# Optimization experiments

Hardware: AMD Instinct MI355X
Metric: run time of the kernel (lower is better)

## Reference

```python
import jax, jax.numpy as jnp
import numpy as np

B, S, H = 2, 2048, 2048
N_HEADS, N_KV, HEAD_DIM = 16, 8, 128
EPS = 1e-6
ROPE_THETA = 1e6


def _rms_norm(x, w, eps=EPS):
    # per-head RMSNorm over last dim (head_dim), computed in fp32
    xf = x.astype(jnp.float32)
    var = jnp.mean(xf * xf, axis=-1, keepdims=True)
    return (w * (xf * jax.lax.rsqrt(var + eps))).astype(x.dtype)


def _rotate_half(x):
    x1, x2 = jnp.split(x, 2, axis=-1)
    return jnp.concatenate((-x2, x1), axis=-1)


def setup_inputs() -> dict:
    key = jax.random.key(0)
    ks = jax.random.split(key, 6)
    hidden_states = jax.random.normal(ks[0], (B, S, H), dtype=jnp.float32)
    # RoPE tables: [B, S, head_dim]
    inv_freq = 1.0 / (ROPE_THETA ** (np.arange(0, HEAD_DIM, 2, dtype=np.float32) / HEAD_DIM))
    pos = np.arange(S, dtype=np.float32)
    freqs = np.outer(pos, inv_freq)                      # [S, head_dim/2]
    emb = np.concatenate([freqs, freqs], axis=-1)        # [S, head_dim]
    cos = jnp.broadcast_to(jnp.asarray(np.cos(emb)), (B, S, HEAD_DIM))
    sin = jnp.broadcast_to(jnp.asarray(np.sin(emb)), (B, S, HEAD_DIM))
    # additive causal mask [B, 1, S, S]
    causal = jnp.triu(jnp.full((S, S), -1e9, dtype=jnp.float32), k=1)
    attention_mask = jnp.broadcast_to(causal[None, None], (B, 1, S, S))
    scale = 0.02
    Wq = jax.random.normal(ks[1], (N_HEADS * HEAD_DIM, H), dtype=jnp.float32) * scale
    Wk = jax.random.normal(ks[2], (N_KV * HEAD_DIM, H), dtype=jnp.float32) * scale
    Wv = jax.random.normal(ks[3], (N_KV * HEAD_DIM, H), dtype=jnp.float32) * scale
    Wo = jax.random.normal(ks[4], (H, N_HEADS * HEAD_DIM), dtype=jnp.float32) * scale
    q_norm_w = jnp.ones((HEAD_DIM,), dtype=jnp.float32)
    k_norm_w = jnp.ones((HEAD_DIM,), dtype=jnp.float32)
    return dict(hidden_states=hidden_states, cos=cos, sin=sin,
                attention_mask=attention_mask, Wq=Wq, Wk=Wk, Wv=Wv, Wo=Wo,
                q_norm_w=q_norm_w, k_norm_w=k_norm_w)


def reference(hidden_states, cos, sin, attention_mask, Wq, Wk, Wv, Wo, q_norm_w, k_norm_w):
    b, s, _ = hidden_states.shape
    scaling = HEAD_DIM ** -0.5
    n_rep = N_HEADS // N_KV
    # QKV projections (torch Linear: x @ W.T), split into heads
    q = jnp.einsum('bsh,dh->bsd', hidden_states, Wq).reshape(b, s, N_HEADS, HEAD_DIM)
    k = jnp.einsum('bsh,dh->bsd', hidden_states, Wk).reshape(b, s, N_KV, HEAD_DIM)
    v = jnp.einsum('bsh,dh->bsd', hidden_states, Wv).reshape(b, s, N_KV, HEAD_DIM)
    # per-head QK RMSNorm, then [B, H, S, D]
    q = _rms_norm(q, q_norm_w).transpose(0, 2, 1, 3)
    k = _rms_norm(k, k_norm_w).transpose(0, 2, 1, 3)
    v = v.transpose(0, 2, 1, 3)
    # RoPE (cos/sin unsqueezed over head dim)
    c = cos[:, None, :, :]
    sn = sin[:, None, :, :]
    q = q * c + _rotate_half(q) * sn
    k = k * c + _rotate_half(k) * sn
    # GQA: repeat kv heads
    k = jnp.repeat(k, n_rep, axis=1)
    v = jnp.repeat(v, n_rep, axis=1)
    # eager attention: materialize full [B, H, S, S] scores
    attn_weights = jnp.einsum('bhqd,bhkd->bhqk', q, k) * scaling + attention_mask
    attn_weights = jax.nn.softmax(attn_weights.astype(jnp.float32), axis=-1).astype(q.dtype)
    attn_output = jnp.einsum('bhqk,bhkd->bhqd', attn_weights, v)
    attn_output = attn_output.transpose(0, 2, 1, 3).reshape(b, s, N_HEADS * HEAD_DIM)
    attn_output = jnp.einsum('bsd,hd->bsh', attn_output, Wo)
    return attn_output, attn_weights
```

## Files before the change

kernel.cpp:

```cpp
#include <hip/hip_runtime.h>
#include <stdint.h>

typedef unsigned short u16;
typedef __attribute__((ext_vector_type(8))) short bf16x8;
typedef __attribute__((ext_vector_type(4))) float f32x4;
typedef __attribute__((ext_vector_type(4))) unsigned short u16x4;
typedef __attribute__((ext_vector_type(8))) unsigned short u16x8;

#define SCALE_LOG2E 0.12751743007633614f

__device__ __forceinline__ u16 f2bf(float x){
  uint32_t u = __float_as_uint(x);
  u += 0x7FFFu + ((u >> 16) & 1u);
  return (u16)(u >> 16);
}
__device__ __forceinline__ u16 f2bf_trunc(float x){
  return (u16)(__float_as_uint(x) >> 16);
}
__device__ __forceinline__ float bf2f(u16 h){
  return __uint_as_float(((uint32_t)h) << 16);
}
__device__ __forceinline__ void gload16(const void* g, void* l){
  __builtin_amdgcn_global_load_lds((const __attribute__((address_space(1))) void*)g,
                                   (__attribute__((address_space(3))) void*)l, 16, 0, 0);
}

__global__ __launch_bounds__(256) void k_cvt5(
    const float* __restrict__ s0, u16* __restrict__ d0,
    const float* __restrict__ s1, u16* __restrict__ d1,
    const float* __restrict__ s2, u16* __restrict__ d2,
    const float* __restrict__ s3, u16* __restrict__ d3,
    const float* __restrict__ s4, u16* __restrict__ d4)
{
  int b = blockIdx.x;
  const float* s; u16* d; int off;
  if      (b < 8192)  { s=s0; d=d0; off=b; }
  else if (b < 12288) { s=s1; d=d1; off=b-8192; }
  else if (b < 14336) { s=s2; d=d2; off=b-12288; }
  else if (b < 16384) { s=s3; d=d3; off=b-14336; }
  else                { s=s4; d=d4; off=b-16384; }
  size_t i = ((size_t)off * 256 + threadIdx.x) * 4;
  float4 v = *(const float4*)(s + i);
  ushort4 o;
  o.x = f2bf(v.x); o.y = f2bf(v.y); o.z = f2bf(v.z); o.w = f2bf(v.w);
  *(ushort4*)(d + i) = o;
}

#define STAGE_UNIT(PTR, ROWOFF, BUF, TENS, KS, T1) do{ \
  _Pragma("unroll") \
  for(int jj=0;jj<2;jj++){ \
    int rs_ = wid*32 + jj*16 + (lane>>2); \
    int kp_ = (lane&3) ^ ((rs_>>1)&3); \
    gload16((PTR) + (size_t)((ROWOFF)+rs_)*K + (size_t)(T1)*64 + (KS)*32 + kp_*8, \
            &lds[BUF][TENS][KS][(wid*2+jj)*512]); \
  }}while(0)

#define FRAG(BASE, ROW) (*(const bf16x8*)((BASE) + (ROW)*32 + ((c_ ^ (((ROW)>>1)&3))<<3)))

__global__ __launch_bounds__(512,2) void k_gemm256(
    const u16* __restrict__ A, const u16* __restrict__ Bw, void* __restrict__ Cout,
    int N, int K, int ldc, int out_f32)
{
  __shared__ u16 lds[2][2][2][256*32];
  const int tid = threadIdx.x, wid = tid>>6, lane = tid&63;
  const int nbn = N >> 8;
  const int cpx = gridDim.x >> 3;
  const int bid = (blockIdx.x & 7)*cpx + (blockIdx.x >> 3);
  const int bm = bid / nbn, bn = bid % nbn;
  const int m0 = bm<<8, n0 = bn<<8;
  const int wm = wid>>2, wn = wid&3;
  const int c_ = lane>>4, rl = lane&15;

  f32x4 acc[8][4];
  f32x4 zero4 = {0.f,0.f,0.f,0.f};
#pragma unroll
  for (int i=0;i<8;i++)
#pragma unroll
    for (int j=0;j<4;j++) acc[i][j] = zero4;

  STAGE_UNIT(A,  m0, 0, 0, 0, 0);
  STAGE_UNIT(Bw, n0, 0, 1, 0, 0);
  STAGE_UNIT(A,  m0, 0, 0, 1, 0);
  STAGE_UNIT(Bw, n0, 0, 1, 1, 0);

  const int nt = K >> 6;
#pragma unroll 2
  for (int t=0; t<nt; ++t) {
    const int cur = t&1, nxt = cur^1;
    const bool pf = (t+1 < nt);
    const u16* Ab0 = lds[cur][0][0];
    const u16* Bb0 = lds[cur][1][0];
    const u16* Ab1 = lds[cur][0][1];
    const u16* Bb1 = lds[cur][1][1];
    bf16x8 af[4], bf[4];

    asm volatile("s_waitcnt vmcnt(4)" ::: "memory");
    __builtin_amdgcn_s_barrier();
    asm volatile("" ::: "memory");
#pragma unroll
    for (int j=0;j<4;j++) bf[j] = FRAG(Bb0, wn*64 + j*16 + rl);
#pragma unroll
    for (int i=0;i<4;i++) af[i] = FRAG(Ab0, wm*128 + i*16 + rl);
    if (pf) STAGE_UNIT(A, m0, nxt, 0, 0, t+1);
    __builtin_amdgcn_s_setprio(1);
#pragma unroll
    for (int i=0;i<4;i++)
#pragma unroll
      for (int j=0;j<4;j++)
        acc[i][j] = __builtin_amdgcn_mfma_f32_16x16x32_bf16(af[i], bf[j], acc[i][j], 0,0,0);
    __builtin_amdgcn_s_setprio(0);
    __builtin_amdgcn_s_barrier();
    asm volatile("" ::: "memory");

#pragma unroll
    for (int i=0;i<4;i++) af[i] = FRAG(Ab0, wm*128 + (i+4)*16 + rl);
    if (pf) STAGE_UNIT(Bw, n0, nxt, 1, 0, t+1);
    __builtin_amdgcn_s_setprio(1);
#pragma unroll
    for (int i=0;i<4;i++)
#pragma unroll
      for (int j=0;j<4;j++)
        acc[i+4][j] = __builtin_amdgcn_mfma_f32_16x16x32_bf16(af[i], bf[j], acc[i+4][j], 0,0,0);
    __builtin_amdgcn_s_setprio(0);
    __builtin_amdgcn_s_barrier();
    asm volatile("" ::: "memory");

    if (pf) { asm volatile("s_waitcnt vmcnt(4)" ::: "memory"); }
    else    { asm volatile("s_waitcnt vmcnt(0)" ::: "memory"); }
    __builtin_amdgcn_s_barrier();
    asm volatile("" ::: "memory");
#pragma unroll
    for (int j=0;j<4;j++) bf[j] = FRAG(Bb1, wn*64 + j*16 + rl);
#pragma unroll
    for (int i=0;i<4;i++) af[i] = FRAG(Ab1, wm*128 + i*16 + rl);
    if (pf) STAGE_UNIT(A, m0, nxt, 0, 1, t+1);
    __builtin_amdgcn_s_setprio(1);
#pragma unroll
    for (int i=0;i<4;i++)
#pragma unroll
      for (int j=0;j<4;j++)
        acc[i][j] = __builtin_amdgcn_mfma_f32_16x16x32_bf16(af[i], bf[j], acc[i][j], 0,0,0);
    __builtin_amdgcn_s_setprio(0);
    __builtin_amdgcn_s_barrier();
    asm volatile("" ::: "memory");

#pragma unroll
    for (int i=0;i<4;i++) af[i] = FRAG(Ab1, wm*128 + (i+4)*16 + rl);
    if (pf) STAGE_UNIT(Bw, n0, nxt, 1, 1, t+1);
    __builtin_amdgcn_s_setprio(1);
#pragma unroll
    for (int i=0;i<4;i++)
#pragma unroll
      for (int j=0;j<4;j++)
        acc[i+4][j] = __builtin_amdgcn_mfma_f32_16x16x32_bf16(af[i], bf[j], acc[i+4][j], 0,0,0);
    __builtin_amdgcn_s_setprio(0);
    __builtin_amdgcn_s_barrier();
    asm volatile("" ::: "memory");
  }

  const int r0 = m0 + wm*128 + ((lane>>4)<<2);
  const int c0 = n0 + wn*64 + rl;
  if (out_f32) {
    float* C = (float*)Cout;
#pragma unroll
    for (int i=0;i<8;i++)
#pragma unroll
      for (int j=0;j<4;j++)
#pragma unroll
        for (int r=0;r<4;r++)
          C[(size_t)(r0 + i*16 + r)*ldc + (c0 + j*16)] = acc[i][j][r];
  } else {
    u16* C = (u16*)Cout;
#pragma unroll
    for (int i=0;i<8;i++)
#pragma unroll
      for (int j=0;j<4;j++)
#pragma unroll
        for (int r=0;r<4;r++)
          C[(size_t)(r0 + i*16 + r)*ldc + (c0 + j*16)] = f2bf(acc[i][j][r]);
  }
}

#define STAGE_A128(BUF, KS, T1) do{ \
  int rs_ = wid*16 + (lane>>2); \
  int kp_ = (lane&3) ^ ((rs_>>1)&3); \
  gload16(A + (size_t)(m0+rs_)*K + (size_t)(T1)*64 + (KS)*32 + kp_*8, \
          &ldsA[BUF][KS][wid*512]); \
  }while(0)

#define STAGE_B128(BUF, KS, T1) do{ \
  _Pragma("unroll") \
  for(int jj=0;jj<2;jj++){ \
    int rs_ = wid*32 + jj*16 + (lane>>2); \
    int kp_ = (lane&3) ^ ((rs_>>1)&3); \
    gload16(Bw + (size_t)(n0+rs_)*K + (size_t)(T1)*64 + (KS)*32 + kp_*8, \
            &ldsB[BUF][KS][(wid*2+jj)*512]); \
  }}while(0)

__global__ __launch_bounds__(512,2) void k_gemm_bm128(
    const u16* __restrict__ A, const u16* __restrict__ Bw, float* __restrict__ C,
    int N, int K, int ldc)
{
  __shared__ u16 ldsA[2][2][128*32];
  __shared__ u16 ldsB[2][2][256*32];
  const int tid = threadIdx.x, wid = tid>>6, lane = tid&63;
  const int nbn = N >> 8;
  const int cpx = gridDim.x >> 3;
  const int bid = (blockIdx.x & 7)*cpx + (blockIdx.x >> 3);
  const int bm = bid / nbn, bn = bid % nbn;
  const int m0 = bm<<7, n0 = bn<<8;
  const int wm = wid>>2, wn = wid&3;
  const int c_ = lane>>4, rl = lane&15;

  f32x4 acc[4][4];
  f32x4 zero4 = {0.f,0.f,0.f,0.f};
#pragma unroll
  for (int i=0;i<4;i++)
#pragma unroll
    for (int j=0;j<4;j++) acc[i][j] = zero4;

  STAGE_A128(0, 0, 0);
  STAGE_B128(0, 0, 0);
  STAGE_A128(0, 1, 0);
  STAGE_B128(0, 1, 0);

  const int nt = K >> 6;
#pragma unroll 2
  for (int t=0; t<nt; ++t) {
    const int cur = t&1, nxt = cur^1;
    const bool pf = (t+1 < nt);
    bf16x8 af[4], bf[4];

    asm volatile("s_waitcnt vmcnt(3)" ::: "memory");
    __builtin_amdgcn_s_barrier();
    asm volatile("" ::: "memory");
#pragma unroll
    for (int i=0;i<4;i++) af[i] = FRAG(ldsA[cur][0], wm*64 + i*16 + rl);
#pragma unroll
    for (int j=0;j<4;j++) bf[j] = FRAG(ldsB[cur][0], wn*64 + j*16 + rl);
    if (pf) { STAGE_A128(nxt, 0, t+1); STAGE_B128(nxt, 0, t+1); }
    __builtin_amdgcn_s_setprio(1);
#pragma unroll
    for (int i=0;i<4;i++)
#pragma unroll
      for (int j=0;j<4;j++)
        acc[i][j] = __builtin_amdgcn_mfma_f32_16x16x32_bf16(af[i], bf[j], acc[i][j], 0,0,0);
    __builtin_amdgcn_s_setprio(0);
    __builtin_amdgcn_s_barrier();
    asm volatile("" ::: "memory");

    if (pf) { asm volatile("s_waitcnt vmcnt(3)" ::: "memory"); }
    else    { asm volatile("s_waitcnt vmcnt(0)" ::: "memory"); }
    __builtin_amdgcn_s_barrier();
    asm volatile("" ::: "memory");
#pragma unroll
    for (int i=0;i<4;i++) af[i] = FRAG(ldsA[cur][1], wm*64 + i*16 + rl);
#pragma unroll
    for (int j=0;j<4;j++) bf[j] = FRAG(ldsB[cur][1], wn*64 + j*16 + rl);
    if (pf) { STAGE_A128(nxt, 1, t+1); STAGE_B128(nxt, 1, t+1); }
    __builtin_amdgcn_s_setprio(1);
#pragma unroll
    for (int i=0;i<4;i++)
#pragma unroll
      for (int j=0;j<4;j++)
        acc[i][j] = __builtin_amdgcn_mfma_f32_16x16x32_bf16(af[i], bf[j], acc[i][j], 0,0,0);
    __builtin_amdgcn_s_setprio(0);
    __builtin_amdgcn_s_barrier();
    asm volatile("" ::: "memory");
  }

  const int r0 = m0 + wm*64 + ((lane>>4)<<2);
  const int c0 = n0 + wn*64 + rl;
#pragma unroll
  for (int i=0;i<4;i++)
#pragma unroll
    for (int j=0;j<4;j++)
#pragma unroll
      for (int r=0;r<4;r++)
        C[(size_t)(r0 + i*16 + r)*ldc + (c0 + j*16)] = acc[i][j][r];
}

__global__ __launch_bounds__(256) void k_prep(
    u16* __restrict__ qkv, u16* __restrict__ vt,
    const float* __restrict__ cosb, const float* __restrict__ sinb,
    const float* __restrict__ kw)
{
  __shared__ u16 tile[64][72];
  const int tid = threadIdx.x;
  if (blockIdx.x < 8192) {
    const int lane = tid&63;
    const int task = blockIdx.x*4 + (tid>>6);
    const int bs = task >> 3, col = 2048 + (task & 7)*128;
    u16* row = qkv + (size_t)bs*4096 + col;
    float x0 = bf2f(row[lane]), x1 = bf2f(row[lane+64]);
    float ss = x0*x0 + x1*x1;
#pragma unroll
    for (int m=1; m<64; m<<=1) ss += __shfl_xor(ss, m, 64);
    float rn = rsqrtf(ss*(1.0f/128.0f) + 1e-6f);
    const float* cp = cosb + (size_t)bs*128;
    const float* sp = sinb + (size_t)bs*128;
    float q0 = x0*rn*kw[lane], q1 = x1*rn*kw[lane+64];
    float o0 = q0*cp[lane]    - q1*sp[lane];
    float o1 = q1*cp[lane+64] + q0*sp[lane+64];
    row[lane]    = f2bf(o0);
    row[lane+64] = f2bf(o1);
  } else {
    const int bid = blockIdx.x - 8192;
    const int dt = bid & 1, st = (bid>>1)&31, kvh = (bid>>6)&7, b = bid>>9;
    const int rr = tid >> 3, c = (tid & 7) * 8;
    const u16* src = qkv + ((size_t)(b*2048 + st*64))*4096 + 3072 + kvh*128 + dt*64;
#pragma unroll
    for (int p=0;p<2;p++){
      int sl = p*32 + rr;
      u16x8 v = *(const u16x8*)(src + (size_t)sl*4096 + c);
#pragma unroll
      for (int e=0;e<8;e++) tile[sl][c+e] = v[e];
    }
    __syncthreads();
    u16* dst = vt + ((size_t)((b*8+kvh)*128 + dt*64))*2048 + st*64;
#pragma unroll
    for (int p=0;p<2;p++){
      int dl = p*32 + rr;
      u16x8 o;
#pragma unroll
      for (int e=0;e<8;e++) o[e] = tile[c+e][dl];
      *(u16x8*)(dst + (size_t)dl*2048 + c) = o;
    }
  }
}

#define STAGE_K8(T, DSTBUF) do { \
  _Pragma("unroll") \
  for (int i_=0;i_<2;i_++){ \
    int r_ = wv*8 + i_*4 + (lane>>4); \
    int cs_ = (lane&15) ^ (r_&7); \
    gload16(Kb + (size_t)((T)*64 + r_)*4096 + cs_*8, (DSTBUF) + (wv*2+i_)*512); \
  } } while(0)

#define STAGE_V8(T, DSTBUF) do { \
  _Pragma("unroll") \
  for (int i_=0;i_<2;i_++){ \
    int d_ = wv*16 + i_*8 + (lane>>3); \
    int cs_ = (lane&7) ^ (d_&7); \
    gload16(Vb + (size_t)d_*2048 + (T)*64 + cs_*8, (DSTBUF) + (wv*2+i_)*512); \
  } } while(0)

#define COMPUTE_S16(SACC, KBUF) do { \
  _Pragma("unroll") \
  for (int ks_=0;ks_<4;ks_++){ \
    bf16x8 bfr_[4]; \
    _Pragma("unroll") \
    for (int ns_=0;ns_<4;ns_++){ \
      int n_ = ns_*16 + (lane&15); \
      int sl_ = (ks_*4 + (lane>>4)) ^ (n_&7); \
      bfr_[ns_] = *(const bf16x8*)((KBUF) + n_*128 + sl_*8); \
    } \
    _Pragma("unroll") \
    for (int ns_=0;ns_<4;ns_++) \
      SACC[ns_] = __builtin_amdgcn_mfma_f32_16x16x32_bf16(qf[ks_], bfr_[ns_], SACC[ns_], 0,0,0); \
  } } while(0)

__global__ __launch_bounds__(512,4) void k_attn(
    const u16* __restrict__ qkv, const u16* __restrict__ vt,
    const float* __restrict__ cosb, const float* __restrict__ sinb,
    const float* __restrict__ qw,
    float* __restrict__ probs, u16* __restrict__ attn_o)
{
  __shared__ u16 lKV[4][64*128];
  __shared__ u16 lP[8][16*64];
  const int tid = threadIdx.x, wv = tid>>6, lane = tid&63;
  const int rl = lane&15, hi = lane>>4;
  const int bid = blockIdx.x;
  const int r9 = bid >> 5;
  const int qt = (r9 < 8) ? (15 - r9) : (r9 - 8);
  const int bh = bid & 31;
  const int h = bh & 15, b = bh >> 4;
  const int kvh = h>>1;
  const int q0 = qt<<7;
  const u16* Qb = qkv + (size_t)b*2048*4096 + h*128;
  const u16* Kb = qkv + (size_t)b*2048*4096 + 2048 + kvh*128;
  const u16* Vb = vt + (size_t)(b*8+kvh)*128*2048;

  f32x4 zero4 = {0.f,0.f,0.f,0.f};

  const int nkt = 2*qt + 2;
  const int tdiag = 2*qt + (wv>>2);
  const int rb = q0 + wv*16 + hi*4;

  STAGE_K8(0, lKV[0]);
  STAGE_K8(1, lKV[1]);
  if (nkt > 2) STAGE_K8(2, lKV[2]);

  bf16x8 qf[4];
  {
    const int srow = q0 + wv*16 + rl;
    float xq[4][8];
    float ss = 0.f;
#pragma unroll
    for (int ks=0;ks<4;ks++){
      bf16x8 raw = *(const bf16x8*)(Qb + (size_t)srow*4096 + ks*32 + hi*8);
#pragma unroll
      for (int j=0;j<8;j++){
        float x = bf2f((u16)raw[j]);
        xq[ks][j] = x;
        ss += x*x;
      }
    }
    ss += __shfl_xor(ss, 16, 64);
    ss += __shfl_xor(ss, 32, 64);
    float rn = rsqrtf(ss*(1.0f/128.0f) + 1e-6f);
    const float* cp = cosb + (size_t)(b*2048 + srow)*128;
    const float* sp = sinb + (size_t)(b*2048 + srow)*128;
#pragma unroll
    for (int ks2=0;ks2<2;ks2++){
#pragma unroll
      for (int j=0;j<8;j++){
        int d0 = ks2*32 + hi*8 + j;
        int d1 = d0 + 64;
        float a  = xq[ks2][j]   * rn * qw[d0];
        float bb = xq[ks2+2][j] * rn * qw[d1];
        float o0 = a*cp[d0] - bb*sp[d0];
        float o1 = bb*cp[d1] + a*sp[d1];
        qf[ks2][j]   = (short)f2bf(o0);
        qf[ks2+2][j] = (short)f2bf(o1);
      }
    }
  }

  float lsum[4] = {0.f,0.f,0.f,0.f};

  for (int t=0; t<nkt; ++t) {
    if      (t+2 < nkt) { asm volatile("s_waitcnt vmcnt(4)" ::: "memory"); }
    else if (t+1 < nkt) { asm volatile("s_waitcnt vmcnt(2)" ::: "memory"); }
    else                { asm volatile("s_waitcnt vmcnt(0)" ::: "memory"); }
    __syncthreads();
    if (t+3 < nkt) STAGE_K8(t+3, lKV[(t+3)&3]);
    asm volatile("" ::: "memory");
    if (t <= tdiag) {
      f32x4 sacc[4];
#pragma unroll
      for (int ns=0;ns<4;ns++) sacc[ns] = zero4;
      COMPUTE_S16(sacc, lKV[t&3]);
      const int cb = t*64 + rl;
      if (t == tdiag) {
#pragma unroll
        for (int ns=0;ns<4;ns++)
#pragma unroll
          for (int r=0;r<4;r++){
            int rg = rb + r, cg = cb + ns*16;
            float e = __builtin_exp2f(sacc[ns][r]*SCALE_LOG2E);
            lsum[r] += (cg <= rg) ? e : 0.f;
          }
      } else {
#pragma unroll
        for (int ns=0;ns<4;ns++)
#pragma unroll
          for (int r=0;r<4;r++)
            lsum[r] += __builtin_exp2f(sacc[ns][r]*SCALE_LOG2E);
      }
    }
  }
#pragma unroll
  for (int m=1;m<16;m<<=1)
#pragma unroll
    for (int r=0;r<4;r++) lsum[r] += __shfl_xor(lsum[r], m, 64);
  float Lr[4];
#pragma unroll
  for (int r=0;r<4;r++) Lr[r] = -__log2f(lsum[r]);

  f32x4 oacc[8];
#pragma unroll
  for (int nd=0;nd<8;nd++) oacc[nd] = zero4;

  u16* pw = lP[wv];
  float* pb = probs + (size_t)bh*2048*2048;

  int cur = 0;
  STAGE_K8(0, lKV[0]);
  STAGE_V8(0, lKV[2]);
  asm volatile("s_waitcnt vmcnt(0)" ::: "memory");
  __syncthreads();
  for (int t=0; t<nkt; ++t) {
    const bool pf = (t+1 < nkt);
    if (pf) { STAGE_K8(t+1, lKV[cur^1]); STAGE_V8(t+1, lKV[2+(cur^1)]); }
    asm volatile("" ::: "memory");
    if (t <= tdiag) {
      f32x4 sacc[4];
#pragma unroll
      for (int ns=0;ns<4;ns++) sacc[ns] = zero4;
      COMPUTE_S16(sacc, lKV[cur]);
      const int cb = t*64 + rl;
      if (t == tdiag) {
#pragma unroll
        for (int ns=0;ns<4;ns++)
#pragma unroll
          for (int r=0;r<4;r++){
            int rg = rb + r, cg = cb + ns*16;
            float p = (cg <= rg) ? __builtin_exp2f(fmaf(sacc[ns][r], SCALE_LOG2E, Lr[r])) : 0.f;
            int ql = hi*4 + r, kl = ns*16 + rl;
            pw[ql*64 + (((kl>>3) ^ (ql&7))<<3) + (kl&7)] = f2bf_trunc(p);
          }
      } else {
#pragma unroll
        for (int ns=0;ns<4;ns++)
#pragma unroll
          for (int r=0;r<4;r++){
            float p = __builtin_exp2f(fmaf(sacc[ns][r], SCALE_LOG2E, Lr[r]));
            int ql = hi*4 + r, kl = ns*16 + rl;
            pw[ql*64 + (((kl>>3) ^ (ql&7))<<3) + (kl&7)] = f2bf_trunc(p);
          }
      }
      {
        const int cq = rl, grp = cq>>1, off = (cq&1)*4;
#pragma unroll
        for (int it=0; it<4; ++it){
          int row = it*4 + hi;
          int slot = grp ^ (row&7);
          u16x4 pk4 = *(const u16x4*)(pw + row*64 + slot*8 + off);
          f32x4 pf4;
#pragma unroll
          for (int r=0;r<4;r++) pf4[r] = bf2f(pk4[r]);
          __builtin_nontemporal_store(pf4,
            (f32x4*)(pb + (size_t)(q0 + wv*16 + row)*2048 + t*64 + cq*4));
        }
      }
      const u16* vbuf = lKV[2+cur];
#pragma unroll
      for (int kks=0;kks<2;kks++){
        bf16x8 pa;
        {
          int ql = rl;
          int sl = (kks*4 + hi) ^ (ql&7);
          pa = *(const bf16x8*)(pw + ql*64 + sl*8);
        }
#pragma unroll
        for (int nd=0;nd<8;nd++){
          int d = nd*16 + rl;
          int sl = (kks*4 + hi) ^ (d&7);
          bf16x8 vb = *(const bf16x8*)(vbuf + d*64 + sl*8);
          oacc[nd] = __builtin_amdgcn_mfma_f32_16x16x32_bf16(pa, vb, oacc[nd], 0,0,0);
        }
      }
    }
    if (pf) {
      asm volatile("s_waitcnt vmcnt(4)" ::: "memory");
      __syncthreads();
    }
    cur ^= 1;
  }

  const int kend = (tdiag+1)*64;
  f32x4 z4 = {0.f,0.f,0.f,0.f};
  for (int q = wv*16; q < wv*16+16; ++q){
    float* rp = pb + (size_t)(q0 + q)*2048;
    for (int c = kend + lane*4; c < 2048; c += 256)
      __builtin_nontemporal_store(z4, (f32x4*)(rp + c));
  }

#pragma unroll
  for (int nd=0;nd<8;nd++)
#pragma unroll
    for (int r=0;r<4;r++){
      int rg = rb + r;
      int cg = h*128 + nd*16 + rl;
      attn_o[(size_t)(b*2048 + rg)*2048 + cg] = f2bf(oacc[nd][r]);
    }
}

extern "C" void kernel_launch(void* const* d_in, const int* in_sizes, int n_in,
                              void* d_out, int out_size, void* d_ws, size_t ws_size,
                              hipStream_t stream) {
  (void)in_sizes; (void)n_in; (void)out_size; (void)ws_size;
  const float* hs   = (const float*)d_in[0];
  const float* cosb = (const float*)d_in[1];
  const float* sinb = (const float*)d_in[2];
  const float* Wq   = (const float*)d_in[4];
  const float* Wk   = (const float*)d_in[5];
  const float* Wv   = (const float*)d_in[6];
  const float* Wo   = (const float*)d_in[7];
  const float* qw   = (const float*)d_in[8];
  const float* kw   = (const float*)d_in[9];
  float* out   = (float*)d_out;
  float* probs = out + 8388608;

  char* ws = (char*)d_ws;
  u16* hs_b   = (u16*)(ws);
  u16* attn_o = hs_b;
  u16* W_all  = (u16*)(ws + (16u<<20));
  u16* Wo_b   = (u16*)(ws + (32u<<20));
  u16* qkv    = (u16*)(ws + (40u<<20));
  u16* v_t    = (u16*)(ws + (72u<<20));

  k_cvt5<<<20480,256,0,stream>>>(hs, hs_b, Wq, W_all, Wk, W_all + 4194304,
                                 Wv, W_all + 6291456, Wo, Wo_b);

  k_gemm256<<<256,512,0,stream>>>(hs_b, W_all, (void*)qkv, 4096, 2048, 4096, 0);
  k_prep<<<9216,256,0,stream>>>(qkv, v_t, cosb, sinb, kw);
  k_attn<<<512,512,0,stream>>>(qkv, v_t, cosb, sinb, qw, probs, attn_o);
  k_gemm_bm128<<<256,512,0,stream>>>(attn_o, Wo_b, out, 2048, 2048, 2048);
}
```

Before: 311.4 us.

## Swap QK MFMA operands so each lane owns a query row

The QK^T MFMA now takes K as the A operand and Q as the B operand, so each lane holds four consecutive key columns for one query row. The row sum becomes a single scalar per lane, reduced with two shuffles instead of sixteen. The fp32 probability tile is now written straight from registers instead of being round-tripped through LDS as bf16, and the bf16 P tile goes to LDS with vector stores instead of scalar ones. In exchange, each row's global probability write covers 64 contiguous bytes instead of 256, which may coalesce worse. The stored probabilities are also no longer truncated to bf16 first.

```diff
diff --git a/kernel.cpp b/kernel.cpp
--- a/kernel.cpp
+++ b/kernel.cpp
@@ -345,19 +345,19 @@
     gload16(Vb + (size_t)d_*2048 + (T)*64 + cs_*8, (DSTBUF) + (wv*2+i_)*512); \
   } } while(0)
 
-#define COMPUTE_S16(SACC, KBUF) do { \
+#define COMPUTE_S16_SW(SACC, KBUF) do { \
   _Pragma("unroll") \
   for (int ks_=0;ks_<4;ks_++){ \
-    bf16x8 bfr_[4]; \
+    bf16x8 kfr_[4]; \
     _Pragma("unroll") \
     for (int ns_=0;ns_<4;ns_++){ \
       int n_ = ns_*16 + (lane&15); \
       int sl_ = (ks_*4 + (lane>>4)) ^ (n_&7); \
-      bfr_[ns_] = *(const bf16x8*)((KBUF) + n_*128 + sl_*8); \
+      kfr_[ns_] = *(const bf16x8*)((KBUF) + n_*128 + sl_*8); \
     } \
     _Pragma("unroll") \
     for (int ns_=0;ns_<4;ns_++) \
-      SACC[ns_] = __builtin_amdgcn_mfma_f32_16x16x32_bf16(qf[ks_], bfr_[ns_], SACC[ns_], 0,0,0); \
+      SACC[ns_] = __builtin_amdgcn_mfma_f32_16x16x32_bf16(kfr_[ns_], qf[ks_], SACC[ns_], 0,0,0); \
   } } while(0)
 
 __global__ __launch_bounds__(512,4) void k_attn(
@@ -385,6 +385,7 @@
 
   const int nkt = 2*qt + 2;
   const int tdiag = 2*qt + (wv>>2);
+  const int rq = q0 + wv*16 + rl;
   const int rb = q0 + wv*16 + hi*4;
 
   STAGE_K8(0, lKV[0]);
@@ -393,12 +394,11 @@
 
   bf16x8 qf[4];
   {
-    const int srow = q0 + wv*16 + rl;
     float xq[4][8];
     float ss = 0.f;
 #pragma unroll
     for (int ks=0;ks<4;ks++){
-      bf16x8 raw = *(const bf16x8*)(Qb + (size_t)srow*4096 + ks*32 + hi*8);
+      bf16x8 raw = *(const bf16x8*)(Qb + (size_t)rq*4096 + ks*32 + hi*8);
 #pragma unroll
       for (int j=0;j<8;j++){
         float x = bf2f((u16)raw[j]);
@@ -409,8 +409,8 @@
     ss += __shfl_xor(ss, 16, 64);
     ss += __shfl_xor(ss, 32, 64);
     float rn = rsqrtf(ss*(1.0f/128.0f) + 1e-6f);
-    const float* cp = cosb + (size_t)(b*2048 + srow)*128;
-    const float* sp = sinb + (size_t)(b*2048 + srow)*128;
+    const float* cp = cosb + (size_t)(b*2048 + rq)*128;
+    const float* sp = sinb + (size_t)(b*2048 + rq)*128;
 #pragma unroll
     for (int ks2=0;ks2<2;ks2++){
 #pragma unroll
@@ -427,7 +427,7 @@
     }
   }
 
-  float lsum[4] = {0.f,0.f,0.f,0.f};
+  float lsum = 0.f;
 
   for (int t=0; t<nkt; ++t) {
     if      (t+2 < nkt) { asm volatile("s_waitcnt vmcnt(4)" ::: "memory"); }
@@ -440,33 +440,28 @@
       f32x4 sacc[4];
 #pragma unroll
       for (int ns=0;ns<4;ns++) sacc[ns] = zero4;
-      COMPUTE_S16(sacc, lKV[t&3]);
-      const int cb = t*64 + rl;
+      COMPUTE_S16_SW(sacc, lKV[t&3]);
       if (t == tdiag) {
 #pragma unroll
         for (int ns=0;ns<4;ns++)
 #pragma unroll
           for (int r=0;r<4;r++){
-            int rg = rb + r, cg = cb + ns*16;
+            int cg = t*64 + ns*16 + hi*4 + r;
             float e = __builtin_exp2f(sacc[ns][r]*SCALE_LOG2E);
-            lsum[r] += (cg <= rg) ? e : 0.f;
+            lsum += (cg <= rq) ? e : 0.f;
           }
       } else {
 #pragma unroll
         for (int ns=0;ns<4;ns++)
 #pragma unroll
           for (int r=0;r<4;r++)
-            lsum[r] += __builtin_exp2f(sacc[ns][r]*SCALE_LOG2E);
+            lsum += __builtin_exp2f(sacc[ns][r]*SCALE_LOG2E);
       }
     }
   }
-#pragma unroll
-  for (int m=1;m<16;m<<=1)
-#pragma unroll
-    for (int r=0;r<4;r++) lsum[r] += __shfl_xor(lsum[r], m, 64);
-  float Lr[4];
-#pragma unroll
-  for (int r=0;r<4;r++) Lr[r] = -__log2f(lsum[r]);
+  lsum += __shfl_xor(lsum, 16, 64);
+  lsum += __shfl_xor(lsum, 32, 64);
+  const float Lr = -__log2f(lsum);
 
   f32x4 oacc[8];
 #pragma unroll
@@ -474,6 +469,7 @@
 
   u16* pw = lP[wv];
   float* pb = probs + (size_t)bh*2048*2048;
+  float* prow = pb + (size_t)rq*2048 + hi*4;
 
   int cur = 0;
   STAGE_K8(0, lKV[0]);
@@ -488,50 +484,36 @@
       f32x4 sacc[4];
 #pragma unroll
       for (int ns=0;ns<4;ns++) sacc[ns] = zero4;
-      COMPUTE_S16(sacc, lKV[cur]);
-      const int cb = t*64 + rl;
-      if (t == tdiag) {
-#pragma unroll
-        for (int ns=0;ns<4;ns++)
+      COMPUTE_S16_SW(sacc, lKV[cur]);
+#pragma unroll
+      for (int ns=0;ns<4;ns++){
+        f32x4 pv;
+        if (t == tdiag) {
+          const int cg0 = t*64 + ns*16 + hi*4;
 #pragma unroll
           for (int r=0;r<4;r++){
-            int rg = rb + r, cg = cb + ns*16;
-            float p = (cg <= rg) ? __builtin_exp2f(fmaf(sacc[ns][r], SCALE_LOG2E, Lr[r])) : 0.f;
-            int ql = hi*4 + r, kl = ns*16 + rl;
-            pw[ql*64 + (((kl>>3) ^ (ql&7))<<3) + (kl&7)] = f2bf_trunc(p);
+            float e = __builtin_exp2f(fmaf(sacc[ns][r], SCALE_LOG2E, Lr));
+            pv[r] = (cg0 + r <= rq) ? e : 0.f;
           }
-      } else {
-#pragma unroll
-        for (int ns=0;ns<4;ns++)
-#pragma unroll
-          for (int r=0;r<4;r++){
-            float p = __builtin_exp2f(fmaf(sacc[ns][r], SCALE_LOG2E, Lr[r]));
-            int ql = hi*4 + r, kl = ns*16 + rl;
-            pw[ql*64 + (((kl>>3) ^ (ql&7))<<3) + (kl&7)] = f2bf_trunc(p);
-          }
-      }
-      {
-        const int cq = rl, grp = cq>>1, off = (cq&1)*4;
-#pragma unroll
-        for (int it=0; it<4; ++it){
-          int row = it*4 + hi;
-          int slot = grp ^ (row&7);
-          u16x4 pk4 = *(const u16x4*)(pw + row*64 + slot*8 + off);
-          f32x4 pf4;
-#pragma unroll
-          for (int r=0;r<4;r++) pf4[r] = bf2f(pk4[r]);
-          __builtin_nontemporal_store(pf4,
-            (f32x4*)(pb + (size_t)(q0 + wv*16 + row)*2048 + t*64 + cq*4));
+        } else {
+#pragma unroll
+          for (int r=0;r<4;r++)
+            pv[r] = __builtin_exp2f(fmaf(sacc[ns][r], SCALE_LOG2E, Lr));
         }
+        __builtin_nontemporal_store(pv, (f32x4*)(prow + t*64 + ns*16));
+        u16x4 pk;
+#pragma unroll
+        for (int r=0;r<4;r++) pk[r] = f2bf_trunc(pv[r]);
+        const int slot = (ns*2 + (hi>>1)) ^ (rl&7);
+        *(u16x4*)(pw + rl*64 + slot*8 + (hi&1)*4) = pk;
       }
       const u16* vbuf = lKV[2+cur];
 #pragma unroll
       for (int kks=0;kks<2;kks++){
         bf16x8 pa;
         {
-          int ql = rl;
-          int sl = (kks*4 + hi) ^ (ql&7);
-          pa = *(const bf16x8*)(pw + ql*64 + sl*8);
+          const int sl = (kks*4 + hi) ^ (rl&7);
+          pa = *(const bf16x8*)(pw + rl*64 + sl*8);
         }
 #pragma unroll
         for (int nd=0;nd<8;nd++){
```

Result: slower. 338.0 us (+8.5%).
